# Optimization experiments

Measured on AMD Instinct MI355X. Metric: run time of the kernel, lower is better.

Reference implementation:

```python
import jax, jax.numpy as jnp
import numpy as np

N, D, E = 100000, 128, 800000

def setup_inputs() -> dict:
    key = jax.random.key(0)
    k1, k2, k3, k4 = jax.random.split(key, 4)
    z = jax.random.normal(k1, (N, D), dtype=jnp.float32)
    edge_index = jax.random.randint(k2, (2, E), 0, N, dtype=jnp.int64)
    # PyTorch-style init scale for Linear layers (kaiming-uniform-ish via normal is fine for a numeric reference)
    W1 = jax.random.normal(k3, (2 * D, D), dtype=jnp.float32) * (1.0 / np.sqrt(2 * D))
    b1 = jnp.zeros((D,), dtype=jnp.float32)
    W2 = jax.random.normal(k4, (D, 1), dtype=jnp.float32) * (1.0 / np.sqrt(D))
    b2 = jnp.zeros((1,), dtype=jnp.float32)
    return {"z": z, "edge_index": edge_index, "W1": W1, "b1": b1, "W2": W2, "b2": b2}

def reference(z, edge_index, W1, b1, W2, b2):
    # row/col gather of node embeddings
    row, col = edge_index[0], edge_index[1]
    # cat([z[row], z[col]]) @ W1 == z[row] @ W1[:D] + z[col] @ W1[D:]
    # -> avoids materializing the [E, 2D] concatenated tensor
    d = z.shape[1]
    h = z[row] @ W1[:d] + z[col] @ W1[d:] + b1          # [E, D]
    h = jax.nn.relu(h)                                   # Dropout(0.1) is identity in eval mode
    out = h @ W2 + b2                                    # [E, 1]
    return out.squeeze(-1)                               # [E]
```

## Files before the change

### kernel.cpp

```cpp
#include <hip/hip_runtime.h>

#define DDIM 128

typedef __bf16 bf16x8 __attribute__((ext_vector_type(8)));
typedef float  floatx4 __attribute__((ext_vector_type(4)));

__device__ inline unsigned short f2bf(float f) {
    unsigned u = __builtin_bit_cast(unsigned, f);
    u += 0x7fffu + ((u >> 16) & 1u);
    return (unsigned short)(u >> 16);
}
__device__ inline float bf2f(unsigned short s) {
    unsigned u = ((unsigned)s) << 16;
    return __builtin_bit_cast(float, u);
}

#define EPI_STRIDE 132

__global__ __launch_bounds__(256) void precompute_uv_mfma(
    const float* __restrict__ z, const float* __restrict__ W1,
    const float* __restrict__ b1,
    unsigned short* __restrict__ U, unsigned short* __restrict__ V,
    int N, int nchunks)
{
    __shared__ unsigned short WsF[32 * 64 * 8];
    __shared__ unsigned short epi[64 * EPI_STRIDE];

    const int t    = threadIdx.x;
    const int lane = t & 63;
    const int w    = t >> 6;
    const int half = blockIdx.x;
    unsigned short* __restrict__ dst = half ? V : U;
    const float* __restrict__ Wh = W1 + (size_t)half * DDIM * DDIM;

    {
        const int nlow = lane & 15;
        const int kq   = (lane >> 4) & 3;
        #pragma unroll
        for (int i = 0; i < 8; ++i) {
            const int ntks = w + i * 4;
            const int nt = ntks >> 2, ks = ntks & 3;
            const int n  = nt * 16 + nlow;
            const int kb = ks * 32 + kq * 8;
            unsigned short frag[8];
            #pragma unroll
            for (int j = 0; j < 8; ++j)
                frag[j] = f2bf(Wh[(kb + j) * DDIM + n]);
            *(uint4*)&WsF[(ntks * 64 + lane) * 8] = *(const uint4*)frag;
        }
    }
    __syncthreads();

    const int mrow = lane & 15;
    const int quad = lane >> 4;

    for (int chunk = blockIdx.y; chunk < nchunks; chunk += gridDim.y) {
        const int m0 = chunk * 64 + w * 16;

        bf16x8 afrag[4];
        {
            int grow = m0 + mrow; if (grow > N - 1) grow = N - 1;
            const float* zrow = z + (size_t)grow * DDIM;
            #pragma unroll
            for (int ks = 0; ks < 4; ++ks) {
                const int k0 = ks * 32 + quad * 8;
                const float4 x0 = *(const float4*)(zrow + k0);
                const float4 x1 = *(const float4*)(zrow + k0 + 4);
                unsigned short a[8];
                a[0] = f2bf(x0.x); a[1] = f2bf(x0.y); a[2] = f2bf(x0.z); a[3] = f2bf(x0.w);
                a[4] = f2bf(x1.x); a[5] = f2bf(x1.y); a[6] = f2bf(x1.z); a[7] = f2bf(x1.w);
                afrag[ks] = __builtin_bit_cast(bf16x8, *(const uint4*)a);
            }
        }

        floatx4 acc[8];
        #pragma unroll
        for (int nt = 0; nt < 8; ++nt) acc[nt] = (floatx4){0.f, 0.f, 0.f, 0.f};

        #pragma unroll
        for (int ks = 0; ks < 4; ++ks) {
            #pragma unroll
            for (int nt = 0; nt < 8; ++nt) {
                const bf16x8 b = __builtin_bit_cast(bf16x8,
                    *(const uint4*)&WsF[((nt * 4 + ks) * 64 + lane) * 8]);
                acc[nt] = __builtin_amdgcn_mfma_f32_16x16x32_bf16(afrag[ks], b, acc[nt], 0, 0, 0);
            }
        }

        #pragma unroll
        for (int nt = 0; nt < 8; ++nt) {
            const int col  = nt * 16 + mrow;
            const float bias = (half == 0) ? b1[col] : 0.f;
            #pragma unroll
            for (int r = 0; r < 4; ++r) {
                const int lrow = w * 16 + quad * 4 + r;
                epi[lrow * EPI_STRIDE + col] = f2bf(acc[nt][r] + bias);
            }
        }
        __builtin_amdgcn_s_waitcnt(0);

        {
            const int cg = lane & 31;
            const int r2 = lane >> 5;
            #pragma unroll
            for (int it = 0; it < 8; ++it) {
                const int lr   = r2 + it * 2;
                const int lrow = w * 16 + lr;
                const uint2 dat = *(const uint2*)&epi[lrow * EPI_STRIDE + cg * 4];
                const int grow = chunk * 64 + lrow;
                if (grow < N)
                    *(uint2*)&dst[(size_t)grow * DDIM + cg * 4] = dat;
            }
        }
        __syncthreads();
    }
}

__global__ __launch_bounds__(256) void edge_kernel_bf16(
    const int* __restrict__ ei,
    const unsigned short* __restrict__ U, const unsigned short* __restrict__ V,
    const float* __restrict__ W2, const float* __restrict__ b2,
    float* __restrict__ out, int E)
{
    const int t  = threadIdx.x;
    const int p  = t & 15;
    const int g0 = (blockIdx.x * 16 + (t >> 4)) * 4;

    float ww[8];
    {
        const float4 w0 = *(const float4*)(W2 + p * 8);
        const float4 w4 = *(const float4*)(W2 + p * 8 + 4);
        ww[0]=w0.x; ww[1]=w0.y; ww[2]=w0.z; ww[3]=w0.w;
        ww[4]=w4.x; ww[5]=w4.y; ww[6]=w4.z; ww[7]=w4.w;
    }

    if (g0 >= E) return;

    int rows[4], cols[4];
    if (g0 + 3 < E) {
        const int4 r4 = *(const int4*)(ei + g0);
        const int4 c4 = *(const int4*)(ei + (size_t)E + g0);
        rows[0]=r4.x; rows[1]=r4.y; rows[2]=r4.z; rows[3]=r4.w;
        cols[0]=c4.x; cols[1]=c4.y; cols[2]=c4.z; cols[3]=c4.w;
    } else {
        #pragma unroll
        for (int i = 0; i < 4; ++i) {
            const int gi = (g0 + i < E) ? (g0 + i) : (E - 1);
            rows[i] = ei[gi];
            cols[i] = ei[(size_t)E + gi];
        }
    }

    uint4 uu[4], vv[4];
    #pragma unroll
    for (int i = 0; i < 4; ++i)
        uu[i] = *(const uint4*)(U + (size_t)rows[i] * DDIM + p * 8);
    #pragma unroll
    for (int i = 0; i < 4; ++i)
        vv[i] = *(const uint4*)(V + (size_t)cols[i] * DDIM + p * 8);

    const float bias = b2[0];

    #pragma unroll
    for (int i = 0; i < 4; ++i) {
        const unsigned short* us = (const unsigned short*)&uu[i];
        const unsigned short* vs = (const unsigned short*)&vv[i];
        float s = 0.f;
        #pragma unroll
        for (int j = 0; j < 8; ++j) {
            const float h = bf2f(us[j]) + bf2f(vs[j]);
            s = fmaf(fmaxf(h, 0.f), ww[j], s);
        }
        #pragma unroll
        for (int off = 8; off > 0; off >>= 1)
            s += __shfl_down(s, off, 16);
        if (p == 0 && g0 + i < E) out[g0 + i] = s + bias;
    }
}

__global__ __launch_bounds__(256) void edge_fused_fallback(
    const float* __restrict__ z, const int* __restrict__ ei,
    const float* __restrict__ W1, const float* __restrict__ b1,
    const float* __restrict__ W2, const float* __restrict__ b2,
    float* __restrict__ out, int N, int E)
{
    const int tid  = blockIdx.x * 256 + threadIdx.x;
    const int e    = tid >> 6;
    const int lane = tid & 63;
    if (e >= E) return;

    const int row = ei[e];
    const int col = ei[(size_t)E + e];
    const float* zr = z + (size_t)row * DDIM;
    const float* zc = z + (size_t)col * DDIM;

    float h0 = b1[lane];
    float h1 = b1[lane + 64];
    for (int k = 0; k < DDIM; ++k) {
        const float a = zr[k];
        const float b = zc[k];
        h0 = fmaf(a, W1[k * DDIM + lane],               h0);
        h0 = fmaf(b, W1[(DDIM + k) * DDIM + lane],      h0);
        h1 = fmaf(a, W1[k * DDIM + lane + 64],          h1);
        h1 = fmaf(b, W1[(DDIM + k) * DDIM + lane + 64], h1);
    }
    float s = fmaxf(h0, 0.f) * W2[lane] + fmaxf(h1, 0.f) * W2[lane + 64];
    #pragma unroll
    for (int off = 32; off > 0; off >>= 1)
        s += __shfl_down(s, off, 64);
    if (lane == 0) out[e] = s + b2[0];
}

extern "C" void kernel_launch(void* const* d_in, const int* in_sizes, int n_in,
                              void* d_out, int out_size, void* d_ws, size_t ws_size,
                              hipStream_t stream)
{
    const float* z  = (const float*)d_in[0];
    const int*   ei = (const int*)d_in[1];
    const float* W1 = (const float*)d_in[2];
    const float* b1 = (const float*)d_in[3];
    const float* W2 = (const float*)d_in[4];
    const float* b2 = (const float*)d_in[5];
    float*       out = (float*)d_out;

    const int N = in_sizes[0] / DDIM;
    const int E = in_sizes[1] / 2;

    const size_t uv_bytes = 2 * (size_t)N * DDIM * sizeof(unsigned short);
    if (ws_size >= uv_bytes) {
        unsigned short* U = (unsigned short*)d_ws;
        unsigned short* V = U + (size_t)N * DDIM;
        const int nchunks = (N + 63) / 64;
        hipLaunchKernelGGL(precompute_uv_mfma, dim3(2, 384), dim3(256), 0, stream,
                           z, W1, b1, U, V, N, nchunks);
        hipLaunchKernelGGL(edge_kernel_bf16, dim3((E + 63) / 64), dim3(256), 0, stream,
                           ei, U, V, W2, b2, out, E);
    } else {
        hipLaunchKernelGGL(edge_fused_fallback, dim3((E + 3) / 4), dim3(256), 0, stream,
                           z, ei, W1, b1, W2, b2, out, N, E);
    }
}
```

Before: 168.3 us.

## Quantize precomputed U/V projections to int8 with per-row scales

Stores the per-node projections U and V as int8 with a per-row float scale instead of bf16. This halves the bytes gathered per edge in the edge kernel, which is bound by random memory access. The epilogue now does a row max-reduction via shuffles and permutes columns into byte layout. It also drops the trailing __syncthreads since each wave only touches its own rows of shared memory. The cost is a larger quantization error, which may exceed the test tolerance.

```diff
diff --git a/kernel.cpp b/kernel.cpp
--- a/kernel.cpp
+++ b/kernel.cpp
@@ -10,28 +10,26 @@
     u += 0x7fffu + ((u >> 16) & 1u);
     return (unsigned short)(u >> 16);
 }
-__device__ inline float bf2f(unsigned short s) {
-    unsigned u = ((unsigned)s) << 16;
-    return __builtin_bit_cast(float, u);
-}
-
-#define EPI_STRIDE 132
-
-__global__ __launch_bounds__(256) void precompute_uv_mfma(
+
+#define EPI_B 136
+
+__global__ __launch_bounds__(256) void precompute_uv_mfma_q8(
     const float* __restrict__ z, const float* __restrict__ W1,
     const float* __restrict__ b1,
-    unsigned short* __restrict__ U, unsigned short* __restrict__ V,
+    signed char* __restrict__ U8, signed char* __restrict__ V8,
+    float* __restrict__ u_scale, float* __restrict__ v_scale,
     int N, int nchunks)
 {
     __shared__ unsigned short WsF[32 * 64 * 8];
-    __shared__ unsigned short epi[64 * EPI_STRIDE];
+    __shared__ __attribute__((aligned(16))) unsigned char epi[64 * EPI_B];
 
     const int t    = threadIdx.x;
     const int lane = t & 63;
     const int w    = t >> 6;
     const int half = blockIdx.x;
-    unsigned short* __restrict__ dst = half ? V : U;
-    const float* __restrict__ Wh = W1 + (size_t)half * DDIM * DDIM;
+    signed char* __restrict__ dst8 = half ? V8 : U8;
+    float*       __restrict__ dscl = half ? v_scale : u_scale;
+    const float* __restrict__ Wh   = W1 + (size_t)half * DDIM * DDIM;
 
     {
         const int nlow = lane & 15;
@@ -53,6 +51,11 @@
 
     const int mrow = lane & 15;
     const int quad = lane >> 4;
+
+    float bval[8];
+    #pragma unroll
+    for (int nt = 0; nt < 8; ++nt)
+        bval[nt] = (half == 0) ? b1[nt * 16 + mrow] : 0.f;
 
     for (int chunk = blockIdx.y; chunk < nchunks; chunk += gridDim.y) {
         const int m0 = chunk * 64 + w * 16;
@@ -88,37 +91,55 @@
         }
 
         #pragma unroll
-        for (int nt = 0; nt < 8; ++nt) {
-            const int col  = nt * 16 + mrow;
-            const float bias = (half == 0) ? b1[col] : 0.f;
-            #pragma unroll
-            for (int r = 0; r < 4; ++r) {
-                const int lrow = w * 16 + quad * 4 + r;
-                epi[lrow * EPI_STRIDE + col] = f2bf(acc[nt][r] + bias);
+        for (int r = 0; r < 4; ++r) {
+            float mx = 0.f;
+            #pragma unroll
+            for (int nt = 0; nt < 8; ++nt)
+                mx = fmaxf(mx, fabsf(acc[nt][r] + bval[nt]));
+            #pragma unroll
+            for (int m = 1; m < 16; m <<= 1)
+                mx = fmaxf(mx, __shfl_xor(mx, m, 16));
+            mx = fmaxf(mx, 1e-20f);
+            const float inv = 127.f / mx;
+
+            unsigned char bytes[8];
+            #pragma unroll
+            for (int nt = 0; nt < 8; ++nt) {
+                const float v = (acc[nt][r] + bval[nt]) * inv;
+                const int q = (int)rintf(v);
+                bytes[nt] = (unsigned char)(q & 0xff);
+            }
+            const int lrow = w * 16 + quad * 4 + r;
+            *(unsigned long long*)&epi[lrow * EPI_B + mrow * 8] =
+                *(const unsigned long long*)bytes;
+
+            if (mrow == 0) {
+                const int grow = chunk * 64 + lrow;
+                if (grow < N) dscl[grow] = mx * (1.f / 127.f);
             }
         }
         __builtin_amdgcn_s_waitcnt(0);
 
         {
-            const int cg = lane & 31;
-            const int r2 = lane >> 5;
-            #pragma unroll
-            for (int it = 0; it < 8; ++it) {
-                const int lr   = r2 + it * 2;
+            const int cg = lane & 15;
+            const int r2 = lane >> 4;
+            #pragma unroll
+            for (int it = 0; it < 4; ++it) {
+                const int lr   = it * 4 + r2;
                 const int lrow = w * 16 + lr;
-                const uint2 dat = *(const uint2*)&epi[lrow * EPI_STRIDE + cg * 4];
+                const uint2 dat = *(const uint2*)&epi[lrow * EPI_B + cg * 8];
                 const int grow = chunk * 64 + lrow;
                 if (grow < N)
-                    *(uint2*)&dst[(size_t)grow * DDIM + cg * 4] = dat;
-            }
-        }
-        __syncthreads();
-    }
-}
-
-__global__ __launch_bounds__(256) void edge_kernel_bf16(
+                    *(uint2*)&dst8[(size_t)grow * DDIM + cg * 8] = dat;
+            }
+        }
+    }
+}
+
+__global__ __launch_bounds__(256) void edge_kernel_i8(
     const int* __restrict__ ei,
-    const unsigned short* __restrict__ U, const unsigned short* __restrict__ V,
+    const signed char* __restrict__ U8, const signed char* __restrict__ V8,
+    const float* __restrict__ u_scale, const float* __restrict__ v_scale,
     const float* __restrict__ W2, const float* __restrict__ b2,
     float* __restrict__ out, int E)
 {
@@ -127,12 +148,8 @@
     const int g0 = (blockIdx.x * 16 + (t >> 4)) * 4;
 
     float ww[8];
-    {
-        const float4 w0 = *(const float4*)(W2 + p * 8);
-        const float4 w4 = *(const float4*)(W2 + p * 8 + 4);
-        ww[0]=w0.x; ww[1]=w0.y; ww[2]=w0.z; ww[3]=w0.w;
-        ww[4]=w4.x; ww[5]=w4.y; ww[6]=w4.z; ww[7]=w4.w;
-    }
+    #pragma unroll
+    for (int j = 0; j < 8; ++j) ww[j] = W2[j * 16 + p];
 
     if (g0 >= E) return;
 
@@ -151,24 +168,28 @@
         }
     }
 
-    uint4 uu[4], vv[4];
+    uint2 uu[4], vv[4];
     #pragma unroll
     for (int i = 0; i < 4; ++i)
-        uu[i] = *(const uint4*)(U + (size_t)rows[i] * DDIM + p * 8);
+        uu[i] = *(const uint2*)(U8 + (size_t)rows[i] * DDIM + p * 8);
     #pragma unroll
     for (int i = 0; i < 4; ++i)
-        vv[i] = *(const uint4*)(V + (size_t)cols[i] * DDIM + p * 8);
+        vv[i] = *(const uint2*)(V8 + (size_t)cols[i] * DDIM + p * 8);
+
+    float su[4], sv[4];
+    #pragma unroll
+    for (int i = 0; i < 4; ++i) { su[i] = u_scale[rows[i]]; sv[i] = v_scale[cols[i]]; }
 
     const float bias = b2[0];
 
     #pragma unroll
     for (int i = 0; i < 4; ++i) {
-        const unsigned short* us = (const unsigned short*)&uu[i];
-        const unsigned short* vs = (const unsigned short*)&vv[i];
+        const signed char* us = (const signed char*)&uu[i];
+        const signed char* vs = (const signed char*)&vv[i];
         float s = 0.f;
         #pragma unroll
         for (int j = 0; j < 8; ++j) {
-            const float h = bf2f(us[j]) + bf2f(vs[j]);
+            const float h = fmaf(sv[i], (float)vs[j], su[i] * (float)us[j]);
             s = fmaf(fmaxf(h, 0.f), ww[j], s);
         }
         #pragma unroll
@@ -226,15 +247,18 @@
     const int N = in_sizes[0] / DDIM;
     const int E = in_sizes[1] / 2;
 
-    const size_t uv_bytes = 2 * (size_t)N * DDIM * sizeof(unsigned short);
-    if (ws_size >= uv_bytes) {
-        unsigned short* U = (unsigned short*)d_ws;
-        unsigned short* V = U + (size_t)N * DDIM;
+    const size_t n128 = (size_t)N * DDIM;
+    const size_t need = 2 * n128 + 2 * (size_t)N * sizeof(float) + 256;
+    if (ws_size >= need) {
+        signed char* U8 = (signed char*)d_ws;
+        signed char* V8 = U8 + n128;
+        float* usc = (float*)(((size_t)(V8 + n128) + 255) & ~(size_t)255);
+        float* vsc = usc + N;
         const int nchunks = (N + 63) / 64;
-        hipLaunchKernelGGL(precompute_uv_mfma, dim3(2, 384), dim3(256), 0, stream,
-                           z, W1, b1, U, V, N, nchunks);
-        hipLaunchKernelGGL(edge_kernel_bf16, dim3((E + 63) / 64), dim3(256), 0, stream,
-                           ei, U, V, W2, b2, out, E);
+        hipLaunchKernelGGL(precompute_uv_mfma_q8, dim3(2, 384), dim3(256), 0, stream,
+                           z, W1, b1, U8, V8, usc, vsc, N, nchunks);
+        hipLaunchKernelGGL(edge_kernel_i8, dim3((E + 63) / 64), dim3(256), 0, stream,
+                           ei, U8, V8, usc, vsc, W2, b2, out, E);
     } else {
         hipLaunchKernelGGL(edge_fused_fallback, dim3((E + 3) / 4), dim3(256), 0, stream,
                            z, ei, W1, b1, W2, b2, out, N, E);
```

New measurement: 140.8 us. 16.4% less time.
